# Kernel optimization log

Measured on AMD Instinct MI355X. Metric: run time of the kernel, lower is better.

Reference implementation:

```python
import jax, jax.numpy as jnp
import numpy as np

NUM_USERS, NUM_ITEMS = 100000, 50000
N_NODES = NUM_USERS + NUM_ITEMS
N_EDGES = 4_000_000
H = 64
BATCH = 100000
MLP_HIDDEN = 32
N_LAYERS = 3


def setup_inputs() -> dict:
    key = jax.random.key(0)
    ks = jax.random.split(key, 12)
    return {
        "edge_index": jax.random.randint(ks[0], (2, N_EDGES), 0, N_NODES, dtype=jnp.int32),
        "user_ids": jax.random.randint(ks[1], (BATCH,), 0, NUM_USERS, dtype=jnp.int32),
        "item_ids": jax.random.randint(ks[2], (BATCH,), 0, NUM_ITEMS, dtype=jnp.int32),
        "user_emb": jax.random.normal(ks[3], (NUM_USERS, H), jnp.float32),
        "item_emb": jax.random.normal(ks[4], (NUM_ITEMS, H), jnp.float32),
        "Wl": jax.random.normal(ks[5], (N_LAYERS, H, H), jnp.float32) * (1.0 / jnp.sqrt(H)),
        "bl": jnp.zeros((N_LAYERS, H), jnp.float32),
        "Wr": jax.random.normal(ks[6], (N_LAYERS, H, H), jnp.float32) * (1.0 / jnp.sqrt(H)),
        "W1": jax.random.normal(ks[7], (2 * H, MLP_HIDDEN), jnp.float32) * (1.0 / jnp.sqrt(2.0 * H)),
        "b1": jnp.zeros((MLP_HIDDEN,), jnp.float32),
        "W2": jax.random.normal(ks[8], (MLP_HIDDEN, 1), jnp.float32) * (1.0 / jnp.sqrt(1.0 * MLP_HIDDEN)),
        "b2": jnp.zeros((1,), jnp.float32),
    }


def _sage_layer(x, src, dst, Wl_i, bl_i, Wr_i):
    # PyG SAGEConv, mean aggr: out = lin_l(mean_{j in N(i)} x_j) + lin_r(x_i)
    msg = x[src]                                                  # [E, H] gather
    summed = jax.ops.segment_sum(msg, dst, num_segments=N_NODES)  # [N, H] scatter-add
    cnt = jax.ops.segment_sum(jnp.ones((src.shape[0],), x.dtype), dst, num_segments=N_NODES)
    mean = summed / jnp.maximum(cnt, 1.0)[:, None]                # empty neighborhoods -> 0
    return mean @ Wl_i + bl_i + x @ Wr_i


def reference(edge_index, user_ids, item_ids, user_emb, item_emb, Wl, bl, Wr, W1, b1, W2, b2):
    src, dst = edge_index[0], edge_index[1]
    x = jnp.concatenate([user_emb, item_emb], axis=0)  # [N, H]
    for l in range(N_LAYERS):
        x = jax.nn.relu(_sage_layer(x, src, dst, Wl[l], bl[l], Wr[l]))
        # dropout is identity in eval mode
    ue = x[user_ids]                   # [B, H]
    ie = x[item_ids + NUM_USERS]       # [B, H]
    pair = jnp.concatenate([ue, ie], axis=-1)  # [B, 2H]
    h = jax.nn.relu(pair @ W1 + b1)
    rating = (h @ W2 + b2)[:, 0]
    return jnp.clip(rating, 1.0, 5.0)
```

## Files before the change

### kernel.cpp

```cpp
#include <hip/hip_runtime.h>
#include <hip/hip_bf16.h>

#define NUM_USERS 100000
#define NUM_ITEMS 50000
#define N_NODES   150000
#define N_EDGES   4000000
#define H         64
#define BATCH     100000
#define MLP_HIDDEN 32
#define NBUCK     586
#define BCAP      8192

typedef unsigned short ushort_t;

__device__ __forceinline__ float bf2f(ushort_t u) {
    return __uint_as_float(((unsigned)u) << 16);
}
__device__ __forceinline__ ushort_t f2bf(float f) {
    unsigned u = __float_as_uint(f);
    u = u + 0x7FFFu + ((u >> 16) & 1u);
    return (ushort_t)(u >> 16);
}
__device__ __forceinline__ float bfLO(unsigned u) { return __uint_as_float(u << 16); }
__device__ __forceinline__ float bfHI(unsigned u) { return __uint_as_float(u & 0xFFFF0000u); }

__global__ __launch_bounds__(256) void init_kernel(const float* __restrict__ ue,
                                                   const float* __restrict__ ie,
                                                   float* __restrict__ x,
                                                   ushort_t* __restrict__ xh) {
    int i = blockIdx.x * 256 + threadIdx.x;
    const int UN4 = NUM_USERS * H / 4;
    float4 v = (i < UN4) ? ((const float4*)ue)[i] : ((const float4*)ie)[i - UN4];
    ((float4*)x)[i] = v;
    uint2 p;
    p.x = (unsigned)f2bf(v.x) | ((unsigned)f2bf(v.y) << 16);
    p.y = (unsigned)f2bf(v.z) | ((unsigned)f2bf(v.w) << 16);
    ((uint2*)xh)[i] = p;
}

#define SCHUNK 4096
#define SPT    (SCHUNK / 256)
__global__ __launch_bounds__(256) void bucket_scatter_kernel(const int* __restrict__ src,
                                                             const int* __restrict__ dst,
                                                             int* __restrict__ bucketCnt,
                                                             int* __restrict__ ebuf) {
    __shared__ int      histL[NBUCK];
    __shared__ int      startL[NBUCK];
    __shared__ int      adjL[NBUCK];
    __shared__ int      curL[NBUCK];
    __shared__ unsigned staged[SCHUNK];
    __shared__ ushort_t sbuck[SCHUNK];

    int t = threadIdx.x;
    int base = blockIdx.x * SCHUNK;
    int nst = min(SCHUNK, N_EDGES - base);

    for (int i = t; i < NBUCK; i += 256) histL[i] = 0;
    __syncthreads();

    int myd[SPT], mys[SPT];
#pragma unroll
    for (int k = 0; k < SPT; ++k) {
        int e = base + k * 256 + t;
        int d = (e < N_EDGES) ? dst[e] : -1;
        mys[k] = (e < N_EDGES) ? src[e] : 0;
        myd[k] = d;
        if (d >= 0) atomicAdd(&histL[d >> 8], 1);
    }
    __syncthreads();

    if (t < 64) {
        const int CH = (NBUCK + 63) / 64;
        int s0 = t * CH;
        int s1 = min(s0 + CH, NBUCK);
        int s = 0;
        for (int i = s0; i < s1; ++i) s += histL[i];
        int v = s;
#pragma unroll
        for (int off = 1; off < 64; off <<= 1) {
            int u = __shfl_up(v, off, 64);
            if (t >= off) v += u;
        }
        int run = v - s;
        for (int i = s0; i < s1; ++i) {
            startL[i] = run;
            run += histL[i];
        }
    }
    __syncthreads();

    for (int b = t; b < NBUCK; b += 256) {
        int h = histL[b];
        int res = h ? (b * BCAP + atomicAdd(&bucketCnt[b], h)) : 0;
        adjL[b] = res - startL[b];
        curL[b] = startL[b];
    }
    __syncthreads();

#pragma unroll
    for (int k = 0; k < SPT; ++k) {
        int d = myd[k];
        if (d >= 0) {
            int b = d >> 8;
            int pos = atomicAdd(&curL[b], 1);
            staged[pos] = ((unsigned)mys[k] << 8) | (unsigned)(d & 255);
            sbuck[pos] = (ushort_t)b;
        }
    }
    __syncthreads();

    for (int i = t; i < nst; i += 256) {
        int b = sbuck[i];
        ebuf[adjL[b] + i] = (int)staged[i];
    }
}

__global__ __launch_bounds__(512) void bucket_build_kernel(const int* __restrict__ ebuf,
                                                           const int* __restrict__ bucketCnt,
                                                           int* __restrict__ deg,
                                                           int* __restrict__ offsets,
                                                           int* __restrict__ csr) {
    __shared__ int degL[256];
    __shared__ int scanL[256];
    __shared__ int curL[256];
    int t = threadIdx.x;
    int b = blockIdx.x;
    int nodeBase = b << 8;
    int start = b * BCAP;
    int cnt = bucketCnt[b];

    if (t < 256) degL[t] = 0;
    __syncthreads();
    for (int i = t; i < cnt; i += 512)
        atomicAdd(&degL[ebuf[start + i] & 255], 1);
    __syncthreads();

    int v = (t < 256) ? degL[t] : 0;
    if (t < 256) scanL[t] = v;
    __syncthreads();
#pragma unroll
    for (int off = 1; off < 256; off <<= 1) {
        int u = (t >= off && t < 256) ? scanL[t - off] : 0;
        __syncthreads();
        if (t < 256) scanL[t] += u;
        __syncthreads();
    }

    if (t < 256) {
        int excl = scanL[t] - v;
        int node = nodeBase + t;
        if (node < N_NODES) {
            deg[node] = v;
            offsets[node] = start + excl;
        }
        curL[t] = excl;
    }
    __syncthreads();

    for (int i = t; i < cnt; i += 512) {
        unsigned p = (unsigned)ebuf[start + i];
        int pos = atomicAdd(&curL[p & 255u], 1);
        csr[start + pos] = (int)(p >> 8);
    }
}

__global__ __launch_bounds__(256, 8) void gather_mean_kernel(const ushort_t* __restrict__ xh,
                                                             ushort_t* __restrict__ mean_bf,
                                                             const int* __restrict__ offsets,
                                                             const int* __restrict__ deg,
                                                             const int* __restrict__ csr) {
    int slot = threadIdx.x >> 6;
    int lane = threadIdx.x & 63;
    int q    = lane >> 4;
    int fp   = lane & 15;
    int node = blockIdx.x * 4 + slot;

    int base = offsets[node];
    int cnt  = deg[node];
    const uint2* xr = (const uint2*)xh;

    float a0 = 0.f, a1 = 0.f, a2 = 0.f, a3 = 0.f;

    for (int c = 0; c < cnt; c += 64) {
        int n = min(64, cnt - c);
        int sid = (c + lane < cnt) ? csr[base + c + lane] : 0;
        int nquad = (n + 3) >> 2;
#define PROC(JJ) { int e = 4 * (JJ) + q;                                  \
        int s = __shfl(sid, e, 64);                                       \
        uint2 u = xr[s * 16 + fp];                                        \
        if (c + e >= cnt) { u.x = 0u; u.y = 0u; }                         \
        a0 += bfLO(u.x); a1 += bfHI(u.x); a2 += bfLO(u.y); a3 += bfHI(u.y); }
        int j = 0;
        for (; j + 2 <= nquad; j += 2) { PROC(j) PROC(j + 1) }
        for (; j < nquad; ++j) { PROC(j) }
#undef PROC
    }

    a0 += __shfl_xor(a0, 16, 64); a1 += __shfl_xor(a1, 16, 64);
    a2 += __shfl_xor(a2, 16, 64); a3 += __shfl_xor(a3, 16, 64);
    a0 += __shfl_xor(a0, 32, 64); a1 += __shfl_xor(a1, 32, 64);
    a2 += __shfl_xor(a2, 32, 64); a3 += __shfl_xor(a3, 32, 64);

    if (lane < 16) {
        float rc = 1.0f / fmaxf((float)cnt, 1.0f);
        uint2 p;
        p.x = (unsigned)f2bf(a0 * rc) | ((unsigned)f2bf(a1 * rc) << 16);
        p.y = (unsigned)f2bf(a2 * rc) | ((unsigned)f2bf(a3 * rc) << 16);
        *(uint2*)&mean_bf[node * H + fp * 4] = p;
    }
}

__global__ __launch_bounds__(256) void transform_kernel(float* __restrict__ x,
                                                        ushort_t* __restrict__ xh,
                                                        const ushort_t* __restrict__ mean_bf,
                                                        const float* __restrict__ Wl,
                                                        const float* __restrict__ bl,
                                                        const float* __restrict__ Wr,
                                                        int writeBf) {
    __shared__ float    sWl[H * H];
    __shared__ float    sWr[H * H];
    __shared__ unsigned sMT[H / 2][128];
    __shared__ unsigned sXT[H / 2][128];

    int t = threadIdx.x;
    int node0 = blockIdx.x * 128;

    for (int i = t; i < H * H / 4; i += 256) {
        ((float4*)sWl)[i] = ((const float4*)Wl)[i];
        ((float4*)sWr)[i] = ((const float4*)Wr)[i];
    }
#pragma unroll
    for (int it = 0; it < 8; ++it) {
        int idx = it * 256 + t;
        int n = idx & 127;
        int qd = idx >> 7;
        int node = node0 + n;
        uint2 mu = make_uint2(0u, 0u);
        uint2 xu = make_uint2(0u, 0u);
        if (node < N_NODES) {
            mu = *(const uint2*)&mean_bf[node * H + qd * 4];
            float4 xv = *(const float4*)&x[node * H + qd * 4];
            xu.x = (unsigned)f2bf(xv.x) | ((unsigned)f2bf(xv.y) << 16);
            xu.y = (unsigned)f2bf(xv.z) | ((unsigned)f2bf(xv.w) << 16);
        }
        sMT[qd * 2][n]     = mu.x;
        sMT[qd * 2 + 1][n] = mu.y;
        sXT[qd * 2][n]     = xu.x;
        sXT[qd * 2 + 1][n] = xu.y;
    }
    __syncthreads();

    int tx = t & 7;
    int ty = t >> 3;
    int nbase = node0 + ty * 4;

    float acc[4][8];
#pragma unroll
    for (int j = 0; j < 4; ++j)
#pragma unroll
        for (int f = 0; f < 8; ++f) acc[j][f] = 0.0f;

    for (int kp = 0; kp < H / 2; ++kp) {
        uint4 mu = *(const uint4*)&sMT[kp][ty * 4];
        uint4 xu = *(const uint4*)&sXT[kp][ty * 4];
        int k0 = kp * 2;
        float4 wl00 = *(const float4*)&sWl[k0 * H + tx * 8];
        float4 wl01 = *(const float4*)&sWl[k0 * H + tx * 8 + 4];
        float4 wr00 = *(const float4*)&sWr[k0 * H + tx * 8];
        float4 wr01 = *(const float4*)&sWr[k0 * H + tx * 8 + 4];
        float4 wl10 = *(const float4*)&sWl[(k0 + 1) * H + tx * 8];
        float4 wl11 = *(const float4*)&sWl[(k0 + 1) * H + tx * 8 + 4];
        float4 wr10 = *(const float4*)&sWr[(k0 + 1) * H + tx * 8];
        float4 wr11 = *(const float4*)&sWr[(k0 + 1) * H + tx * 8 + 4];
        const float wl0[8] = {wl00.x, wl00.y, wl00.z, wl00.w, wl01.x, wl01.y, wl01.z, wl01.w};
        const float wr0[8] = {wr00.x, wr00.y, wr00.z, wr00.w, wr01.x, wr01.y, wr01.z, wr01.w};
        const float wl1[8] = {wl10.x, wl10.y, wl10.z, wl10.w, wl11.x, wl11.y, wl11.z, wl11.w};
        const float wr1[8] = {wr10.x, wr10.y, wr10.z, wr10.w, wr11.x, wr11.y, wr11.z, wr11.w};
        const unsigned mua[4] = {mu.x, mu.y, mu.z, mu.w};
        const unsigned xua[4] = {xu.x, xu.y, xu.z, xu.w};
#pragma unroll
        for (int j = 0; j < 4; ++j) {
            float m0 = bfLO(mua[j]), m1 = bfHI(mua[j]);
            float x0 = bfLO(xua[j]), x1 = bfHI(xua[j]);
#pragma unroll
            for (int f = 0; f < 8; ++f) {
                float a = acc[j][f];
                a = fmaf(m0, wl0[f], a);
                a = fmaf(x0, wr0[f], a);
                a = fmaf(m1, wl1[f], a);
                a = fmaf(x1, wr1[f], a);
                acc[j][f] = a;
            }
        }
    }

    float4 b0 = *(const float4*)&bl[tx * 8];
    float4 b1 = *(const float4*)&bl[tx * 8 + 4];
    const float bias[8] = {b0.x, b0.y, b0.z, b0.w, b1.x, b1.y, b1.z, b1.w};
#pragma unroll
    for (int j = 0; j < 4; ++j) {
        int node = nbase + j;
        if (node < N_NODES) {
            float o[8];
#pragma unroll
            for (int f = 0; f < 8; ++f) o[f] = fmaxf(acc[j][f] + bias[f], 0.0f);
            *(float4*)&x[node * H + tx * 8]     = make_float4(o[0], o[1], o[2], o[3]);
            *(float4*)&x[node * H + tx * 8 + 4] = make_float4(o[4], o[5], o[6], o[7]);
            if (writeBf) {
                uint4 p;
                p.x = (unsigned)f2bf(o[0]) | ((unsigned)f2bf(o[1]) << 16);
                p.y = (unsigned)f2bf(o[2]) | ((unsigned)f2bf(o[3]) << 16);
                p.z = (unsigned)f2bf(o[4]) | ((unsigned)f2bf(o[5]) << 16);
                p.w = (unsigned)f2bf(o[6]) | ((unsigned)f2bf(o[7]) << 16);
                *(uint4*)&xh[node * H + tx * 8] = p;
            }
        }
    }
}

__global__ __launch_bounds__(256) void mlp_kernel(const float* __restrict__ x,
                                                  const int* __restrict__ uids,
                                                  const int* __restrict__ iids,
                                                  const float* __restrict__ W1,
                                                  const float* __restrict__ b1,
                                                  const float* __restrict__ W2,
                                                  const float* __restrict__ b2,
                                                  float* __restrict__ out) {
    __shared__ float sW1[2 * H * MLP_HIDDEN];
    __shared__ float sPair[8][2 * H];
    __shared__ float sW2[MLP_HIDDEN];

    for (int i = threadIdx.x; i < 2 * H * MLP_HIDDEN; i += 256) sW1[i] = W1[i];
    if (threadIdx.x < MLP_HIDDEN) sW2[threadIdx.x] = W2[threadIdx.x];

    int slot = threadIdx.x >> 5;
    int j    = threadIdx.x & 31;
    int b = blockIdx.x * 8 + slot;

    int u  = uids[b];
    int it = iids[b] + NUM_USERS;
    float2 a = *(const float2*)&x[u * H + j * 2];
    sPair[slot][j * 2]     = a.x;
    sPair[slot][j * 2 + 1] = a.y;
    float2 c = *(const float2*)&x[it * H + j * 2];
    sPair[slot][H + j * 2]     = c.x;
    sPair[slot][H + j * 2 + 1] = c.y;
    __syncthreads();

    float hacc = b1[j];
#pragma unroll
    for (int k = 0; k < 2 * H; ++k)
        hacc = fmaf(sPair[slot][k], sW1[k * MLP_HIDDEN + j], hacc);
    hacc = fmaxf(hacc, 0.0f);

    float r = hacc * sW2[j];
#pragma unroll
    for (int off = 16; off; off >>= 1) r += __shfl_down(r, off, 32);

    if (j == 0) out[b] = fminf(fmaxf(r + b2[0], 1.0f), 5.0f);
}

extern "C" void kernel_launch(void* const* d_in, const int* in_sizes, int n_in,
                              void* d_out, int out_size, void* d_ws, size_t ws_size,
                              hipStream_t stream) {
    const int*   edge_index = (const int*)d_in[0];
    const int*   user_ids   = (const int*)d_in[1];
    const int*   item_ids   = (const int*)d_in[2];
    const float* user_emb   = (const float*)d_in[3];
    const float* item_emb   = (const float*)d_in[4];
    const float* Wl         = (const float*)d_in[5];
    const float* bl         = (const float*)d_in[6];
    const float* Wr         = (const float*)d_in[7];
    const float* W1         = (const float*)d_in[8];
    const float* b1         = (const float*)d_in[9];
    const float* W2         = (const float*)d_in[10];
    const float* b2         = (const float*)d_in[11];
    float* out = (float*)d_out;

    const int* src = edge_index;
    const int* dst = edge_index + N_EDGES;

    const size_t NH = (size_t)N_NODES * H;
    float* x          = (float*)d_ws;
    int* ebuf         = (int*)(x + NH);
    ushort_t* mean_bf = (ushort_t*)ebuf;
    ushort_t* xh      = (ushort_t*)(ebuf + (size_t)NBUCK * BCAP);
    int* deg          = (int*)(xh + NH);
    int* offsets      = deg + N_NODES;
    int* bucketCnt    = offsets + N_NODES;
    int* csr          = bucketCnt + NBUCK;

    init_kernel<<<(N_NODES * H / 4) / 256, 256, 0, stream>>>(user_emb, item_emb, x, xh);

    hipMemsetAsync(bucketCnt, 0, NBUCK * sizeof(int), stream);
    bucket_scatter_kernel<<<(N_EDGES + SCHUNK - 1) / SCHUNK, 256, 0, stream>>>(
        src, dst, bucketCnt, ebuf);
    bucket_build_kernel<<<NBUCK, 512, 0, stream>>>(ebuf, bucketCnt, deg, offsets, csr);

    const int TGRID = (N_NODES + 127) / 128;
    for (int l = 0; l < 3; ++l) {
        gather_mean_kernel<<<N_NODES / 4, 256, 0, stream>>>(xh, mean_bf, offsets, deg, csr);
        transform_kernel<<<TGRID, 256, 0, stream>>>(
            x, xh, mean_bf, Wl + (size_t)l * H * H, bl + (size_t)l * H,
            Wr + (size_t)l * H * H, l < 2 ? 1 : 0);
    }

    mlp_kernel<<<BATCH / 8, 256, 0, stream>>>(x, user_ids, item_ids, W1, b1, W2, b2, out);
}
```

Measured before the change: 501.4 us.

## Drop fp32 node features, pad CSR rows with zero-row sentinel, pack FMAs

Removes the fp32 copy of node features entirely, so init, transform and MLP read and write only the bf16 buffer. This cuts the per-layer fp32 read/write traffic. CSR segments are padded to multiples of four with a sentinel index pointing at an all-zero row, which removes the per-edge bounds masking in the gather loop. The transform inner loop uses 2-wide float vectors so the compiler can emit packed FMAs. The trade-off is that the residual path and the MLP inputs now use bf16-rounded features, which lowers accuracy, and the padding adds a few extra gathers of the zero row.

```diff
diff --git a/kernel.cpp b/kernel.cpp
--- a/kernel.cpp
+++ b/kernel.cpp
@@ -10,12 +10,11 @@
 #define MLP_HIDDEN 32
 #define NBUCK     586
 #define BCAP      8192
+#define ZROW      N_NODES
 
 typedef unsigned short ushort_t;
-
-__device__ __forceinline__ float bf2f(ushort_t u) {
-    return __uint_as_float(((unsigned)u) << 16);
-}
+typedef float f32x2 __attribute__((ext_vector_type(2)));
+
 __device__ __forceinline__ ushort_t f2bf(float f) {
     unsigned u = __float_as_uint(f);
     u = u + 0x7FFFu + ((u >> 16) & 1u);
@@ -26,12 +25,10 @@
 
 __global__ __launch_bounds__(256) void init_kernel(const float* __restrict__ ue,
                                                    const float* __restrict__ ie,
-                                                   float* __restrict__ x,
                                                    ushort_t* __restrict__ xh) {
     int i = blockIdx.x * 256 + threadIdx.x;
     const int UN4 = NUM_USERS * H / 4;
     float4 v = (i < UN4) ? ((const float4*)ue)[i] : ((const float4*)ie)[i - UN4];
-    ((float4*)x)[i] = v;
     uint2 p;
     p.x = (unsigned)f2bf(v.x) | ((unsigned)f2bf(v.y) << 16);
     p.y = (unsigned)f2bf(v.z) | ((unsigned)f2bf(v.w) << 16);
@@ -135,8 +132,9 @@
         atomicAdd(&degL[ebuf[start + i] & 255], 1);
     __syncthreads();
 
-    int v = (t < 256) ? degL[t] : 0;
-    if (t < 256) scanL[t] = v;
+    int v  = (t < 256) ? degL[t] : 0;
+    int vp = (v + 3) & ~3;
+    if (t < 256) scanL[t] = vp;
     __syncthreads();
 #pragma unroll
     for (int off = 1; off < 256; off <<= 1) {
@@ -146,8 +144,9 @@
         __syncthreads();
     }
 
+    int excl = 0;
     if (t < 256) {
-        int excl = scanL[t] - v;
+        excl = scanL[t] - vp;
         int node = nodeBase + t;
         if (node < N_NODES) {
             deg[node] = v;
@@ -161,6 +160,11 @@
         unsigned p = (unsigned)ebuf[start + i];
         int pos = atomicAdd(&curL[p & 255u], 1);
         csr[start + pos] = (int)(p >> 8);
+    }
+    __syncthreads();
+
+    if (t < 256) {
+        for (int i = excl + v; i < excl + vp; ++i) csr[start + i] = ZROW;
     }
 }
 
@@ -177,22 +181,21 @@
 
     int base = offsets[node];
     int cnt  = deg[node];
+    int cnt4 = (cnt + 3) & ~3;
     const uint2* xr = (const uint2*)xh;
 
     float a0 = 0.f, a1 = 0.f, a2 = 0.f, a3 = 0.f;
 
-    for (int c = 0; c < cnt; c += 64) {
-        int n = min(64, cnt - c);
-        int sid = (c + lane < cnt) ? csr[base + c + lane] : 0;
-        int nquad = (n + 3) >> 2;
-#define PROC(JJ) { int e = 4 * (JJ) + q;                                  \
-        int s = __shfl(sid, e, 64);                                       \
+    for (int c = 0; c < cnt4; c += 64) {
+        int rem = cnt4 - c;
+        int sid = (lane < rem) ? csr[base + c + lane] : ZROW;
+        int nq = min(64, rem) >> 2;
+#define PROC(JJ) { int s = __shfl(sid, 4 * (JJ) + q, 64);                 \
         uint2 u = xr[s * 16 + fp];                                        \
-        if (c + e >= cnt) { u.x = 0u; u.y = 0u; }                         \
         a0 += bfLO(u.x); a1 += bfHI(u.x); a2 += bfLO(u.y); a3 += bfHI(u.y); }
         int j = 0;
-        for (; j + 2 <= nquad; j += 2) { PROC(j) PROC(j + 1) }
-        for (; j < nquad; ++j) { PROC(j) }
+        for (; j + 2 <= nq; j += 2) { PROC(j) PROC(j + 1) }
+        for (; j < nq; ++j) { PROC(j) }
 #undef PROC
     }
 
@@ -210,13 +213,11 @@
     }
 }
 
-__global__ __launch_bounds__(256) void transform_kernel(float* __restrict__ x,
-                                                        ushort_t* __restrict__ xh,
+__global__ __launch_bounds__(256) void transform_kernel(ushort_t* __restrict__ xh,
                                                         const ushort_t* __restrict__ mean_bf,
                                                         const float* __restrict__ Wl,
                                                         const float* __restrict__ bl,
-                                                        const float* __restrict__ Wr,
-                                                        int writeBf) {
+                                                        const float* __restrict__ Wr) {
     __shared__ float    sWl[H * H];
     __shared__ float    sWr[H * H];
     __shared__ unsigned sMT[H / 2][128];
@@ -239,9 +240,7 @@
         uint2 xu = make_uint2(0u, 0u);
         if (node < N_NODES) {
             mu = *(const uint2*)&mean_bf[node * H + qd * 4];
-            float4 xv = *(const float4*)&x[node * H + qd * 4];
-            xu.x = (unsigned)f2bf(xv.x) | ((unsigned)f2bf(xv.y) << 16);
-            xu.y = (unsigned)f2bf(xv.z) | ((unsigned)f2bf(xv.w) << 16);
+            xu = *(const uint2*)&xh[node * H + qd * 4];
         }
         sMT[qd * 2][n]     = mu.x;
         sMT[qd * 2 + 1][n] = mu.y;
@@ -254,11 +253,11 @@
     int ty = t >> 3;
     int nbase = node0 + ty * 4;
 
-    float acc[4][8];
+    f32x2 acc[4][4];
 #pragma unroll
     for (int j = 0; j < 4; ++j)
 #pragma unroll
-        for (int f = 0; f < 8; ++f) acc[j][f] = 0.0f;
+        for (int p = 0; p < 4; ++p) acc[j][p] = (f32x2)(0.0f);
 
     for (int kp = 0; kp < H / 2; ++kp) {
         uint4 mu = *(const uint4*)&sMT[kp][ty * 4];
@@ -272,53 +271,52 @@
         float4 wl11 = *(const float4*)&sWl[(k0 + 1) * H + tx * 8 + 4];
         float4 wr10 = *(const float4*)&sWr[(k0 + 1) * H + tx * 8];
         float4 wr11 = *(const float4*)&sWr[(k0 + 1) * H + tx * 8 + 4];
-        const float wl0[8] = {wl00.x, wl00.y, wl00.z, wl00.w, wl01.x, wl01.y, wl01.z, wl01.w};
-        const float wr0[8] = {wr00.x, wr00.y, wr00.z, wr00.w, wr01.x, wr01.y, wr01.z, wr01.w};
-        const float wl1[8] = {wl10.x, wl10.y, wl10.z, wl10.w, wl11.x, wl11.y, wl11.z, wl11.w};
-        const float wr1[8] = {wr10.x, wr10.y, wr10.z, wr10.w, wr11.x, wr11.y, wr11.z, wr11.w};
+        f32x2 wl0p[4] = {{wl00.x, wl00.y}, {wl00.z, wl00.w}, {wl01.x, wl01.y}, {wl01.z, wl01.w}};
+        f32x2 wr0p[4] = {{wr00.x, wr00.y}, {wr00.z, wr00.w}, {wr01.x, wr01.y}, {wr01.z, wr01.w}};
+        f32x2 wl1p[4] = {{wl10.x, wl10.y}, {wl10.z, wl10.w}, {wl11.x, wl11.y}, {wl11.z, wl11.w}};
+        f32x2 wr1p[4] = {{wr10.x, wr10.y}, {wr10.z, wr10.w}, {wr11.x, wr11.y}, {wr11.z, wr11.w}};
         const unsigned mua[4] = {mu.x, mu.y, mu.z, mu.w};
         const unsigned xua[4] = {xu.x, xu.y, xu.z, xu.w};
 #pragma unroll
         for (int j = 0; j < 4; ++j) {
-            float m0 = bfLO(mua[j]), m1 = bfHI(mua[j]);
-            float x0 = bfLO(xua[j]), x1 = bfHI(xua[j]);
-#pragma unroll
-            for (int f = 0; f < 8; ++f) {
-                float a = acc[j][f];
-                a = fmaf(m0, wl0[f], a);
-                a = fmaf(x0, wr0[f], a);
-                a = fmaf(m1, wl1[f], a);
-                a = fmaf(x1, wr1[f], a);
-                acc[j][f] = a;
+            f32x2 m0 = (f32x2)(bfLO(mua[j]));
+            f32x2 m1 = (f32x2)(bfHI(mua[j]));
+            f32x2 x0 = (f32x2)(bfLO(xua[j]));
+            f32x2 x1 = (f32x2)(bfHI(xua[j]));
+#pragma unroll
+            for (int p = 0; p < 4; ++p) {
+                f32x2 a = acc[j][p];
+                a = __builtin_elementwise_fma(m0, wl0p[p], a);
+                a = __builtin_elementwise_fma(x0, wr0p[p], a);
+                a = __builtin_elementwise_fma(m1, wl1p[p], a);
+                a = __builtin_elementwise_fma(x1, wr1p[p], a);
+                acc[j][p] = a;
             }
         }
     }
 
     float4 b0 = *(const float4*)&bl[tx * 8];
     float4 b1 = *(const float4*)&bl[tx * 8 + 4];
-    const float bias[8] = {b0.x, b0.y, b0.z, b0.w, b1.x, b1.y, b1.z, b1.w};
+    f32x2 bias[4] = {{b0.x, b0.y}, {b0.z, b0.w}, {b1.x, b1.y}, {b1.z, b1.w}};
 #pragma unroll
     for (int j = 0; j < 4; ++j) {
         int node = nbase + j;
         if (node < N_NODES) {
-            float o[8];
-#pragma unroll
-            for (int f = 0; f < 8; ++f) o[f] = fmaxf(acc[j][f] + bias[f], 0.0f);
-            *(float4*)&x[node * H + tx * 8]     = make_float4(o[0], o[1], o[2], o[3]);
-            *(float4*)&x[node * H + tx * 8 + 4] = make_float4(o[4], o[5], o[6], o[7]);
-            if (writeBf) {
-                uint4 p;
-                p.x = (unsigned)f2bf(o[0]) | ((unsigned)f2bf(o[1]) << 16);
-                p.y = (unsigned)f2bf(o[2]) | ((unsigned)f2bf(o[3]) << 16);
-                p.z = (unsigned)f2bf(o[4]) | ((unsigned)f2bf(o[5]) << 16);
-                p.w = (unsigned)f2bf(o[6]) | ((unsigned)f2bf(o[7]) << 16);
-                *(uint4*)&xh[node * H + tx * 8] = p;
+            uint4 pk;
+            unsigned w[4];
+#pragma unroll
+            for (int p = 0; p < 4; ++p) {
+                float o0 = fmaxf(acc[j][p].x + bias[p].x, 0.0f);
+                float o1 = fmaxf(acc[j][p].y + bias[p].y, 0.0f);
+                w[p] = (unsigned)f2bf(o0) | ((unsigned)f2bf(o1) << 16);
             }
-        }
-    }
-}
-
-__global__ __launch_bounds__(256) void mlp_kernel(const float* __restrict__ x,
+            pk.x = w[0]; pk.y = w[1]; pk.z = w[2]; pk.w = w[3];
+            *(uint4*)&xh[node * H + tx * 8] = pk;
+        }
+    }
+}
+
+__global__ __launch_bounds__(256) void mlp_kernel(const ushort_t* __restrict__ xh,
                                                   const int* __restrict__ uids,
                                                   const int* __restrict__ iids,
                                                   const float* __restrict__ W1,
@@ -339,12 +337,13 @@
 
     int u  = uids[b];
     int it = iids[b] + NUM_USERS;
-    float2 a = *(const float2*)&x[u * H + j * 2];
-    sPair[slot][j * 2]     = a.x;
-    sPair[slot][j * 2 + 1] = a.y;
-    float2 c = *(const float2*)&x[it * H + j * 2];
-    sPair[slot][H + j * 2]     = c.x;
-    sPair[slot][H + j * 2 + 1] = c.y;
+    const uint2* xr = (const uint2*)xh;
+    uint2 v = (j < 16) ? xr[u * 16 + j] : xr[it * 16 + (j - 16)];
+    int off = (j < 16) ? j * 4 : (H + (j - 16) * 4);
+    sPair[slot][off + 0] = bfLO(v.x);
+    sPair[slot][off + 1] = bfHI(v.x);
+    sPair[slot][off + 2] = bfLO(v.y);
+    sPair[slot][off + 3] = bfHI(v.y);
     __syncthreads();
 
     float hacc = b1[j];
@@ -355,7 +354,7 @@
 
     float r = hacc * sW2[j];
 #pragma unroll
-    for (int off = 16; off; off >>= 1) r += __shfl_down(r, off, 32);
+    for (int off2 = 16; off2; off2 >>= 1) r += __shfl_down(r, off2, 32);
 
     if (j == 0) out[b] = fminf(fmaxf(r + b2[0], 1.0f), 5.0f);
 }
@@ -381,16 +380,16 @@
     const int* dst = edge_index + N_EDGES;
 
     const size_t NH = (size_t)N_NODES * H;
-    float* x          = (float*)d_ws;
-    int* ebuf         = (int*)(x + NH);
+    ushort_t* xh      = (ushort_t*)d_ws;
+    int* ebuf         = (int*)(xh + NH + H);
     ushort_t* mean_bf = (ushort_t*)ebuf;
-    ushort_t* xh      = (ushort_t*)(ebuf + (size_t)NBUCK * BCAP);
-    int* deg          = (int*)(xh + NH);
+    int* deg          = ebuf + (size_t)NBUCK * BCAP;
     int* offsets      = deg + N_NODES;
     int* bucketCnt    = offsets + N_NODES;
     int* csr          = bucketCnt + NBUCK;
 
-    init_kernel<<<(N_NODES * H / 4) / 256, 256, 0, stream>>>(user_emb, item_emb, x, xh);
+    init_kernel<<<(N_NODES * H / 4) / 256, 256, 0, stream>>>(user_emb, item_emb, xh);
+    hipMemsetAsync(xh + NH, 0, H * sizeof(ushort_t), stream);
 
     hipMemsetAsync(bucketCnt, 0, NBUCK * sizeof(int), stream);
     bucket_scatter_kernel<<<(N_EDGES + SCHUNK - 1) / SCHUNK, 256, 0, stream>>>(
@@ -401,9 +400,9 @@
     for (int l = 0; l < 3; ++l) {
         gather_mean_kernel<<<N_NODES / 4, 256, 0, stream>>>(xh, mean_bf, offsets, deg, csr);
         transform_kernel<<<TGRID, 256, 0, stream>>>(
-            x, xh, mean_bf, Wl + (size_t)l * H * H, bl + (size_t)l * H,
-            Wr + (size_t)l * H * H, l < 2 ? 1 : 0);
-    }
-
-    mlp_kernel<<<BATCH / 8, 256, 0, stream>>>(x, user_ids, item_ids, W1, b1, W2, b2, out);
-}
+            xh, mean_bf, Wl + (size_t)l * H * H, bl + (size_t)l * H,
+            Wr + (size_t)l * H * H);
+    }
+
+    mlp_kernel<<<BATCH / 8, 256, 0, stream>>>(xh, user_ids, item_ids, W1, b1, W2, b2, out);
+}
```

After: 489.9 us. -2.3%, faster.
